# Kernel tuning notes

Measured on AMD Instinct MI355X. Metric: run time of the kernel, lower is better.

The kernel has to match this reference:

```python
import jax, jax.numpy as jnp
import numpy as np

N, C, M = 4096, 176, 131072   # patches per image, feature dim (32+48+96), memory bank size
CHUNK = 8192                  # memory-bank chunk (torch uses 512; same math, fewer scan steps)
TOPK = 10


def setup_inputs() -> dict:
    key = jax.random.key(0)
    k1, k2 = jax.random.split(key)
    return {
        "patch_feats": jax.random.normal(k1, (N, C), dtype=jnp.float32),
        "memory": jax.random.normal(k2, (M, C), dtype=jnp.float32),
        "topk": TOPK,
    }


def reference(patch_feats, memory, topk):
    eps = 1e-6
    # L2-normalize rows (cosine similarity)
    p = patch_feats / (jnp.linalg.norm(patch_feats, axis=1, keepdims=True) + eps)  # [N, C]
    m = memory / (jnp.linalg.norm(memory, axis=1, keepdims=True) + eps)            # [M, C]

    n_chunks = m.shape[0] // CHUNK
    m_chunks = m.reshape(n_chunks, CHUNK, m.shape[1])  # static chunking of memory bank

    def step(carry_min, mb):
        sim = jnp.einsum('nc,kc->nk', p, mb)       # [N, CHUNK] similarity tile
        d = jnp.min(1.0 - sim, axis=1)             # per-chunk min distance, [N]
        return jnp.minimum(carry_min, d), None

    init = jnp.full((p.shape[0],), jnp.inf, dtype=p.dtype)
    patch_scores, _ = jax.lax.scan(step, init, m_chunks)  # running min over chunks

    # image score: mean of top-k patch scores (topk <= N here)
    topk_vals = jax.lax.top_k(patch_scores, topk)[0]
    image_score = jnp.mean(topk_vals)
    return patch_scores, image_score
```

## Files before the change

### kernel.cpp

```cpp
#include <hip/hip_runtime.h>
#include <stdint.h>

typedef unsigned short ushortT;
typedef __bf16 bf16x8 __attribute__((ext_vector_type(8)));
typedef float f32x4 __attribute__((ext_vector_type(4)));
typedef unsigned short ushort8 __attribute__((ext_vector_type(8)));

#define NPATCH 4096
#define MROWS  131072
#define CFEAT  176
#define KST    6
#define TILE_BYTES 6144
#define MSPLIT 48
#define TOT_ITERS 2048
#define BN_TILES 4
#define ITER_BYTES (BN_TILES * TILE_BYTES)
#define LROW 180

__device__ __forceinline__ ushortT f2bf(float f) {
    unsigned u = __float_as_uint(f);
    unsigned r = (u + 0x7FFFu + ((u >> 16) & 1u)) >> 16;
    return (ushortT)r;
}
__device__ __forceinline__ unsigned f2key(float f) {
    unsigned b = __float_as_uint(f);
    return (b & 0x80000000u) ? ~b : (b | 0x80000000u);
}
__device__ __forceinline__ float key2f(unsigned k) {
    return __uint_as_float((k & 0x80000000u) ? (k ^ 0x80000000u) : ~k);
}

__global__ __launch_bounds__(256) void nrmfrag(const float* __restrict__ in,
                                               ushortT* __restrict__ outfr,
                                               unsigned* __restrict__ keys) {
    __shared__ float buf[64 * LROW];
    __shared__ float scale[64];
    const int t = threadIdx.x;
    const int row0 = blockIdx.x * 64;

    if (keys != nullptr && t < 64) keys[blockIdx.x * 64 + t] = 0u;

    const float4* g4 = reinterpret_cast<const float4*>(in + (size_t)row0 * CFEAT);
#pragma unroll
    for (int i = 0; i < 11; ++i) {
        const int idx = i * 256 + t;
        const int row = idx / 44;
        const int c4  = idx - row * 44;
        float4 v = g4[idx];
        *reinterpret_cast<float4*>(&buf[row * LROW + c4 * 4]) = v;
    }
    __syncthreads();

    {
        const int r = t >> 2, part = t & 3;
        const float* rp = &buf[r * LROW + part * 44];
        float s = 0.f;
#pragma unroll
        for (int i = 0; i < 11; ++i) {
            float4 v = *reinterpret_cast<const float4*>(rp + i * 4);
            s += v.x * v.x + v.y * v.y + v.z * v.z + v.w * v.w;
        }
        s += __shfl_xor(s, 1);
        s += __shfl_xor(s, 2);
        if (part == 0) scale[r] = 1.0f / (sqrtf(s) + 1e-6f);
    }
    __syncthreads();

    const int tl = t >> 6;
    const int lane = t & 63;
    const int col = lane & 15, kh = lane >> 4;
    const int lrow = tl * 16 + col;
    const float* rp = &buf[lrow * LROW];
    const float sc = scale[lrow];
    const size_t tile = (size_t)(row0 >> 4) + tl;
#pragma unroll
    for (int ks = 0; ks < KST; ++ks) {
        const int kb = ks * 32 + kh * 8;
        ushort8 o;
        if (kb < CFEAT) {
            float4 v0 = *reinterpret_cast<const float4*>(rp + kb);
            float4 v1 = *reinterpret_cast<const float4*>(rp + kb + 4);
            o[0] = f2bf(v0.x * sc); o[1] = f2bf(v0.y * sc);
            o[2] = f2bf(v0.z * sc); o[3] = f2bf(v0.w * sc);
            o[4] = f2bf(v1.x * sc); o[5] = f2bf(v1.y * sc);
            o[6] = f2bf(v1.z * sc); o[7] = f2bf(v1.w * sc);
        } else {
#pragma unroll
            for (int j = 0; j < 8; ++j) o[j] = 0;
        }
        *reinterpret_cast<ushort8*>(outfr + (tile * KST + ks) * (size_t)512 + lane * 8) = o;
    }
}

__global__ __launch_bounds__(256, 3) void gemm_max(const ushortT* __restrict__ pfr,
                                                   const ushortT* __restrict__ mfr,
                                                   unsigned* __restrict__ keys) {
    __shared__ ushortT lds[2][ITER_BYTES / 2];
    const int t = threadIdx.x;
    const int w = t >> 6;
    const int lane = t & 63;
    const int mchunk = blockIdx.x;
    const int panel = blockIdx.y;

    const int itb = (mchunk * TOT_ITERS) / MSPLIT;
    const int ite = ((mchunk + 1) * TOT_ITERS) / MSPLIT;

    bf16x8 a[4][KST];
    {
        const int ptile0 = panel * 16 + w * 4;
#pragma unroll
        for (int m = 0; m < 4; ++m)
#pragma unroll
            for (int k = 0; k < KST; ++k)
                a[m][k] = *reinterpret_cast<const bf16x8*>(
                    pfr + ((size_t)(ptile0 + m) * KST + k) * 512 + lane * 8);
    }

    float runmax[4][4];
#pragma unroll
    for (int m = 0; m < 4; ++m)
#pragma unroll
        for (int r = 0; r < 4; ++r) runmax[m][r] = -3.0e38f;

    const uint8_t* gb = reinterpret_cast<const uint8_t*>(mfr);

    auto stage = [&](int buf, int it) {
        const uint8_t* src = gb + (size_t)it * ITER_BYTES + w * 6144 + lane * 16;
        uint8_t* dstb = reinterpret_cast<uint8_t*>(&lds[buf][0]) + w * 6144;
#pragma unroll
        for (int i = 0; i < 6; ++i) {
            __builtin_amdgcn_global_load_lds(
                (const __attribute__((address_space(1))) unsigned int*)(src + i * 1024),
                (__attribute__((address_space(3))) unsigned int*)(dstb + i * 1024),
                16, 0, 0);
        }
    };

    stage(0, itb);
    asm volatile("s_waitcnt vmcnt(0)" ::: "memory");
    __builtin_amdgcn_s_barrier();

    int cur = 0;
    for (int it = itb; it < ite; ++it) {
        if (it + 1 < ite) stage(cur ^ 1, it + 1);

        const ushortT* lb = &lds[cur][0];
#pragma unroll
        for (int n = 0; n < BN_TILES; ++n) {
            bf16x8 b[KST];
#pragma unroll
            for (int k = 0; k < KST; ++k)
                b[k] = *reinterpret_cast<const bf16x8*>(lb + (n * KST + k) * 512 + lane * 8);
            f32x4 acc[4];
#pragma unroll
            for (int m = 0; m < 4; ++m) acc[m] = f32x4{0.f, 0.f, 0.f, 0.f};
#pragma unroll
            for (int k = 0; k < KST; ++k)
#pragma unroll
                for (int m = 0; m < 4; ++m)
                    acc[m] = __builtin_amdgcn_mfma_f32_16x16x32_bf16(a[m][k], b[k], acc[m], 0, 0, 0);
#pragma unroll
            for (int m = 0; m < 4; ++m)
#pragma unroll
                for (int r = 0; r < 4; ++r)
                    runmax[m][r] = fmaxf(runmax[m][r], acc[m][r]);
        }

        asm volatile("s_waitcnt vmcnt(0)" ::: "memory");
        __builtin_amdgcn_s_barrier();
        cur ^= 1;
    }

#pragma unroll
    for (int m = 0; m < 4; ++m) {
#pragma unroll
        for (int r = 0; r < 4; ++r) {
            float v = runmax[m][r];
            v = fmaxf(v, __shfl_xor(v, 1));
            v = fmaxf(v, __shfl_xor(v, 2));
            v = fmaxf(v, __shfl_xor(v, 4));
            v = fmaxf(v, __shfl_xor(v, 8));
            if ((lane & 15) == 0) {
                int prow = panel * 256 + w * 64 + m * 16 + (lane >> 4) * 4 + r;
                atomicMax(&keys[prow], f2key(v));
            }
        }
    }
}

__global__ __launch_bounds__(256) void finalize(const unsigned* __restrict__ keys,
                                                const int* __restrict__ topk_p,
                                                float* __restrict__ out) {
    __shared__ float s[NPATCH];
    __shared__ float rv[256];
    __shared__ int ri[256];
    const int t = threadIdx.x;
    for (int i = t; i < NPATCH; i += 256) {
        float score = 1.0f - key2f(keys[i]);
        out[i] = score;
        s[i] = score;
    }
    __syncthreads();
    const int K = *topk_p;
    float sum = 0.f;
    for (int it = 0; it < K; ++it) {
        float bv = -3.0e38f; int bi = -1;
        for (int i = t; i < NPATCH; i += 256)
            if (s[i] > bv) { bv = s[i]; bi = i; }
        rv[t] = bv; ri[t] = bi;
        __syncthreads();
        for (int off = 128; off > 0; off >>= 1) {
            if (t < off && rv[t + off] > rv[t]) { rv[t] = rv[t + off]; ri[t] = ri[t + off]; }
            __syncthreads();
        }
        if (t == 0) { sum += rv[0]; s[ri[0]] = -3.0e38f; }
        __syncthreads();
    }
    if (t == 0) out[NPATCH] = sum / (float)K;
}

extern "C" void kernel_launch(void* const* d_in, const int* in_sizes, int n_in,
                              void* d_out, int out_size, void* d_ws, size_t ws_size,
                              hipStream_t stream) {
    (void)in_sizes; (void)n_in; (void)out_size; (void)ws_size;
    const float* patch = (const float*)d_in[0];
    const float* mem   = (const float*)d_in[1];
    const int*   topk  = (const int*)d_in[2];
    float* out = (float*)d_out;

    uint8_t* ws = (uint8_t*)d_ws;
    ushortT*  mfr  = (ushortT*)ws;
    ushortT*  pfr  = (ushortT*)(ws + 50331648);
    unsigned* keys = (unsigned*)(ws + 50331648 + 1572864);

    nrmfrag<<<MROWS / 64, 256, 0, stream>>>(mem, mfr, nullptr);
    nrmfrag<<<NPATCH / 64, 256, 0, stream>>>(patch, pfr, keys);
    gemm_max<<<dim3(MSPLIT, NPATCH / 256), 256, 0, stream>>>(pfr, mfr, keys);
    finalize<<<1, 256, 0, stream>>>(keys, topk, out);
}
```

Before: 337.2 us.

## Triple-buffer LDS memory tiles and remap grid for XCD-aware chunk scheduling

Moves the GEMM's memory-bank staging from double to triple buffering. Each iteration now waits with a partial vmcnt so loads run two iterations ahead, and a single barrier per iteration replaces the wait-then-barrier at the loop end. The grid becomes 1D with 32 memory chunks of 64 iterations, and block IDs are swizzled so blocks on the same XCD share M-chunks across patch panels, which should improve L2 reuse. Occupancy drops from 3 to 2 blocks per CU, and fewer chunks means fewer blocks in total (512 instead of 768).

```diff
diff --git a/kernel.cpp b/kernel.cpp
--- a/kernel.cpp
+++ b/kernel.cpp
@@ -11,10 +11,10 @@
 #define CFEAT  176
 #define KST    6
 #define TILE_BYTES 6144
-#define MSPLIT 48
-#define TOT_ITERS 2048
+#define MSPLIT 32
 #define BN_TILES 4
 #define ITER_BYTES (BN_TILES * TILE_BYTES)
+#define ITERS 64
 #define LROW 180
 
 __device__ __forceinline__ ushortT f2bf(float f) {
@@ -92,18 +92,22 @@
     }
 }
 
-__global__ __launch_bounds__(256, 3) void gemm_max(const ushortT* __restrict__ pfr,
+__global__ __launch_bounds__(256, 2) void gemm_max(const ushortT* __restrict__ pfr,
                                                    const ushortT* __restrict__ mfr,
                                                    unsigned* __restrict__ keys) {
-    __shared__ ushortT lds[2][ITER_BYTES / 2];
+    __shared__ ushortT lds[3][ITER_BYTES / 2];
     const int t = threadIdx.x;
     const int w = t >> 6;
     const int lane = t & 63;
-    const int mchunk = blockIdx.x;
-    const int panel = blockIdx.y;
-
-    const int itb = (mchunk * TOT_ITERS) / MSPLIT;
-    const int ite = ((mchunk + 1) * TOT_ITERS) / MSPLIT;
+
+    const int bid = blockIdx.x;
+    const int x = bid & 7;
+    const int slot = bid >> 3;
+    const int mchunk = x + 8 * (slot >> 4);
+    const int panel = slot & 15;
+
+    const int itb = mchunk * ITERS;
+    const int ite = itb + ITERS;
 
     bf16x8 a[4][KST];
     {
@@ -137,14 +141,16 @@
     };
 
     stage(0, itb);
-    asm volatile("s_waitcnt vmcnt(0)" ::: "memory");
-    __builtin_amdgcn_s_barrier();
-
-    int cur = 0;
+    stage(1, itb + 1);
+
+    int cb = 0, sb = 2;
     for (int it = itb; it < ite; ++it) {
-        if (it + 1 < ite) stage(cur ^ 1, it + 1);
-
-        const ushortT* lb = &lds[cur][0];
+        if (it + 1 < ite) asm volatile("s_waitcnt vmcnt(6)" ::: "memory");
+        else              asm volatile("s_waitcnt vmcnt(0)" ::: "memory");
+        __builtin_amdgcn_s_barrier();
+        if (it + 2 < ite) stage(sb, it + 2);
+
+        const ushortT* lb = &lds[cb][0];
 #pragma unroll
         for (int n = 0; n < BN_TILES; ++n) {
             bf16x8 b[KST];
@@ -165,10 +171,8 @@
                 for (int r = 0; r < 4; ++r)
                     runmax[m][r] = fmaxf(runmax[m][r], acc[m][r]);
         }
-
-        asm volatile("s_waitcnt vmcnt(0)" ::: "memory");
-        __builtin_amdgcn_s_barrier();
-        cur ^= 1;
+        cb = (cb == 2) ? 0 : cb + 1;
+        sb = (sb == 2) ? 0 : sb + 1;
     }
 
 #pragma unroll
@@ -235,6 +239,6 @@
 
     nrmfrag<<<MROWS / 64, 256, 0, stream>>>(mem, mfr, nullptr);
     nrmfrag<<<NPATCH / 64, 256, 0, stream>>>(patch, pfr, keys);
-    gemm_max<<<dim3(MSPLIT, NPATCH / 256), 256, 0, stream>>>(pfr, mfr, keys);
+    gemm_max<<<MSPLIT * 16, 256, 0, stream>>>(pfr, mfr, keys);
     finalize<<<1, 256, 0, stream>>>(keys, topk, out);
 }
```

Result: faster. 308.2 us (-8.6%).

## Switch GEMM to 32x32x16 bf16 MFMA with matching fragment layout

Applied to the files above, without the earlier changes.

Replaces the 16x16x32 MFMA tiles with 32x32x16 MFMA tiles. The normalize/fragment kernel now writes data in the 32-row, 16-wide K-step layout, and the GEMM uses 2x2 tiles of 32x32 per wave. The M-split drops from 48 to 32 blocks and the occupancy hint drops from 3 to 2. The larger MFMA shape raises operand reuse per instruction, but it brings heavier register pressure (16-float accumulators and 24 A fragments) and fewer resident blocks.

```diff
diff --git a/kernel.cpp b/kernel.cpp
--- a/kernel.cpp
+++ b/kernel.cpp
@@ -3,18 +3,17 @@
 
 typedef unsigned short ushortT;
 typedef __bf16 bf16x8 __attribute__((ext_vector_type(8)));
-typedef float f32x4 __attribute__((ext_vector_type(4)));
+typedef float f32x16 __attribute__((ext_vector_type(16)));
 typedef unsigned short ushort8 __attribute__((ext_vector_type(8)));
 
 #define NPATCH 4096
 #define MROWS  131072
 #define CFEAT  176
-#define KST    6
-#define TILE_BYTES 6144
-#define MSPLIT 48
-#define TOT_ITERS 2048
-#define BN_TILES 4
-#define ITER_BYTES (BN_TILES * TILE_BYTES)
+#define KS32   12
+#define T32_BYTES 12288
+#define MSPLIT 32
+#define ITER_BYTES 24576
+#define ITERS 64
 #define LROW 180
 
 __device__ __forceinline__ ushortT f2bf(float f) {
@@ -66,16 +65,19 @@
     }
     __syncthreads();
 
-    const int tl = t >> 6;
+    const int p = t >> 7;
+    const int half = (t >> 6) & 1;
     const int lane = t & 63;
-    const int col = lane & 15, kh = lane >> 4;
-    const int lrow = tl * 16 + col;
+    const int rit = lane & 31;
+    const int kh = lane >> 5;
+    const int lrow = p * 32 + rit;
     const float* rp = &buf[lrow * LROW];
     const float sc = scale[lrow];
-    const size_t tile = (size_t)(row0 >> 4) + tl;
-#pragma unroll
-    for (int ks = 0; ks < KST; ++ks) {
-        const int kb = ks * 32 + kh * 8;
+    const size_t tile = (size_t)blockIdx.x * 2 + p;
+#pragma unroll
+    for (int i = 0; i < 6; ++i) {
+        const int ks = half + 2 * i;
+        const int kb = ks * 16 + kh * 8;
         ushort8 o;
         if (kb < CFEAT) {
             float4 v0 = *reinterpret_cast<const float4*>(rp + kb);
@@ -88,11 +90,11 @@
 #pragma unroll
             for (int j = 0; j < 8; ++j) o[j] = 0;
         }
-        *reinterpret_cast<ushort8*>(outfr + (tile * KST + ks) * (size_t)512 + lane * 8) = o;
-    }
-}
-
-__global__ __launch_bounds__(256, 3) void gemm_max(const ushortT* __restrict__ pfr,
+        *reinterpret_cast<ushort8*>(outfr + (tile * KS32 + ks) * (size_t)512 + lane * 8) = o;
+    }
+}
+
+__global__ __launch_bounds__(256, 2) void gemm_max(const ushortT* __restrict__ pfr,
                                                    const ushortT* __restrict__ mfr,
                                                    unsigned* __restrict__ keys) {
     __shared__ ushortT lds[2][ITER_BYTES / 2];
@@ -102,25 +104,25 @@
     const int mchunk = blockIdx.x;
     const int panel = blockIdx.y;
 
-    const int itb = (mchunk * TOT_ITERS) / MSPLIT;
-    const int ite = ((mchunk + 1) * TOT_ITERS) / MSPLIT;
-
-    bf16x8 a[4][KST];
+    const int itb = mchunk * ITERS;
+    const int ite = itb + ITERS;
+
+    bf16x8 a[2][KS32];
     {
-        const int ptile0 = panel * 16 + w * 4;
-#pragma unroll
-        for (int m = 0; m < 4; ++m)
-#pragma unroll
-            for (int k = 0; k < KST; ++k)
+        const int ptile0 = panel * 8 + w * 2;
+#pragma unroll
+        for (int m = 0; m < 2; ++m)
+#pragma unroll
+            for (int k = 0; k < KS32; ++k)
                 a[m][k] = *reinterpret_cast<const bf16x8*>(
-                    pfr + ((size_t)(ptile0 + m) * KST + k) * 512 + lane * 8);
-    }
-
-    float runmax[4][4];
-#pragma unroll
-    for (int m = 0; m < 4; ++m)
-#pragma unroll
-        for (int r = 0; r < 4; ++r) runmax[m][r] = -3.0e38f;
+                    pfr + ((size_t)(ptile0 + m) * KS32 + k) * 512 + lane * 8);
+    }
+
+    float runmax[2][16];
+#pragma unroll
+    for (int m = 0; m < 2; ++m)
+#pragma unroll
+        for (int r = 0; r < 16; ++r) runmax[m][r] = -3.0e38f;
 
     const uint8_t* gb = reinterpret_cast<const uint8_t*>(mfr);
 
@@ -146,23 +148,25 @@
 
         const ushortT* lb = &lds[cur][0];
 #pragma unroll
-        for (int n = 0; n < BN_TILES; ++n) {
-            bf16x8 b[KST];
-#pragma unroll
-            for (int k = 0; k < KST; ++k)
-                b[k] = *reinterpret_cast<const bf16x8*>(lb + (n * KST + k) * 512 + lane * 8);
-            f32x4 acc[4];
-#pragma unroll
-            for (int m = 0; m < 4; ++m) acc[m] = f32x4{0.f, 0.f, 0.f, 0.f};
-#pragma unroll
-            for (int k = 0; k < KST; ++k)
-#pragma unroll
-                for (int m = 0; m < 4; ++m)
-                    acc[m] = __builtin_amdgcn_mfma_f32_16x16x32_bf16(a[m][k], b[k], acc[m], 0, 0, 0);
-#pragma unroll
-            for (int m = 0; m < 4; ++m)
-#pragma unroll
-                for (int r = 0; r < 4; ++r)
+        for (int n = 0; n < 2; ++n) {
+            bf16x8 b[KS32];
+#pragma unroll
+            for (int k = 0; k < KS32; ++k)
+                b[k] = *reinterpret_cast<const bf16x8*>(lb + (n * KS32 + k) * 512 + lane * 8);
+            f32x16 acc[2];
+#pragma unroll
+            for (int m = 0; m < 2; ++m)
+#pragma unroll
+                for (int r = 0; r < 16; ++r) acc[m][r] = 0.f;
+#pragma unroll
+            for (int k = 0; k < KS32; ++k)
+#pragma unroll
+                for (int m = 0; m < 2; ++m)
+                    acc[m] = __builtin_amdgcn_mfma_f32_32x32x16_bf16(a[m][k], b[k], acc[m], 0, 0, 0);
+#pragma unroll
+            for (int m = 0; m < 2; ++m)
+#pragma unroll
+                for (int r = 0; r < 16; ++r)
                     runmax[m][r] = fmaxf(runmax[m][r], acc[m][r]);
         }
 
@@ -172,16 +176,18 @@
     }
 
 #pragma unroll
-    for (int m = 0; m < 4; ++m) {
-#pragma unroll
-        for (int r = 0; r < 4; ++r) {
+    for (int m = 0; m < 2; ++m) {
+#pragma unroll
+        for (int r = 0; r < 16; ++r) {
             float v = runmax[m][r];
             v = fmaxf(v, __shfl_xor(v, 1));
             v = fmaxf(v, __shfl_xor(v, 2));
             v = fmaxf(v, __shfl_xor(v, 4));
             v = fmaxf(v, __shfl_xor(v, 8));
-            if ((lane & 15) == 0) {
-                int prow = panel * 256 + w * 64 + m * 16 + (lane >> 4) * 4 + r;
+            v = fmaxf(v, __shfl_xor(v, 16));
+            if ((lane & 31) == 0) {
+                int rowInTile = (r & 3) + 8 * (r >> 2) + 4 * (lane >> 5);
+                int prow = panel * 256 + w * 64 + m * 32 + rowInTile;
                 atomicMax(&keys[prow], f2key(v));
             }
         }
@@ -235,6 +241,6 @@
 
     nrmfrag<<<MROWS / 64, 256, 0, stream>>>(mem, mfr, nullptr);
     nrmfrag<<<NPATCH / 64, 256, 0, stream>>>(patch, pfr, keys);
-    gemm_max<<<dim3(MSPLIT, NPATCH / 256), 256, 0, stream>>>(pfr, mfr, keys);
+    gemm_max<<<dim3(MSPLIT, 16), 256, 0, stream>>>(pfr, mfr, keys);
     finalize<<<1, 256, 0, stream>>>(keys, topk, out);
 }
```

New measurement: 314.7 us. 1.07x faster.

## Use 512-thread GEMM blocks sharing LDS tiles and a shuffle-based top-k finalize

Applied to the files above, without the earlier changes.

The similarity GEMM now runs 8-wave blocks that each cover 512 patch rows, so every memory-bank tile staged into LDS is reused by twice as many waves. Each wave now issues half as many global-to-LDS loads. The split over the memory bank goes from 48 to 64 chunks of fixed 32 iterations, giving a 64x8 grid. The finalize kernel now keeps its scores in registers across 1024 threads and selects the top-k with wave shuffle reductions instead of an LDS tree with many barriers. In exchange, the larger blocks and higher occupancy target raise register pressure, and the grid has fewer blocks.

```diff
diff --git a/kernel.cpp b/kernel.cpp
--- a/kernel.cpp
+++ b/kernel.cpp
@@ -11,10 +11,10 @@
 #define CFEAT  176
 #define KST    6
 #define TILE_BYTES 6144
-#define MSPLIT 48
-#define TOT_ITERS 2048
+#define MSPLIT 64
 #define BN_TILES 4
 #define ITER_BYTES (BN_TILES * TILE_BYTES)
+#define ITERS 32
 #define LROW 180
 
 __device__ __forceinline__ ushortT f2bf(float f) {
@@ -92,7 +92,7 @@
     }
 }
 
-__global__ __launch_bounds__(256, 3) void gemm_max(const ushortT* __restrict__ pfr,
+__global__ __launch_bounds__(512, 4) void gemm_max(const ushortT* __restrict__ pfr,
                                                    const ushortT* __restrict__ mfr,
                                                    unsigned* __restrict__ keys) {
     __shared__ ushortT lds[2][ITER_BYTES / 2];
@@ -102,12 +102,12 @@
     const int mchunk = blockIdx.x;
     const int panel = blockIdx.y;
 
-    const int itb = (mchunk * TOT_ITERS) / MSPLIT;
-    const int ite = ((mchunk + 1) * TOT_ITERS) / MSPLIT;
+    const int itb = mchunk * ITERS;
+    const int ite = itb + ITERS;
 
     bf16x8 a[4][KST];
     {
-        const int ptile0 = panel * 16 + w * 4;
+        const int ptile0 = panel * 32 + w * 4;
 #pragma unroll
         for (int m = 0; m < 4; ++m)
 #pragma unroll
@@ -125,10 +125,10 @@
     const uint8_t* gb = reinterpret_cast<const uint8_t*>(mfr);
 
     auto stage = [&](int buf, int it) {
-        const uint8_t* src = gb + (size_t)it * ITER_BYTES + w * 6144 + lane * 16;
-        uint8_t* dstb = reinterpret_cast<uint8_t*>(&lds[buf][0]) + w * 6144;
-#pragma unroll
-        for (int i = 0; i < 6; ++i) {
+        const uint8_t* src = gb + (size_t)it * ITER_BYTES + w * 3072 + lane * 16;
+        uint8_t* dstb = reinterpret_cast<uint8_t*>(&lds[buf][0]) + w * 3072;
+#pragma unroll
+        for (int i = 0; i < 3; ++i) {
             __builtin_amdgcn_global_load_lds(
                 (const __attribute__((address_space(1))) unsigned int*)(src + i * 1024),
                 (__attribute__((address_space(3))) unsigned int*)(dstb + i * 1024),
@@ -181,40 +181,57 @@
             v = fmaxf(v, __shfl_xor(v, 4));
             v = fmaxf(v, __shfl_xor(v, 8));
             if ((lane & 15) == 0) {
-                int prow = panel * 256 + w * 64 + m * 16 + (lane >> 4) * 4 + r;
+                int prow = panel * 512 + w * 64 + m * 16 + (lane >> 4) * 4 + r;
                 atomicMax(&keys[prow], f2key(v));
             }
         }
     }
 }
 
-__global__ __launch_bounds__(256) void finalize(const unsigned* __restrict__ keys,
-                                                const int* __restrict__ topk_p,
-                                                float* __restrict__ out) {
-    __shared__ float s[NPATCH];
-    __shared__ float rv[256];
-    __shared__ int ri[256];
+__global__ __launch_bounds__(1024) void finalize(const unsigned* __restrict__ keys,
+                                                 const int* __restrict__ topk_p,
+                                                 float* __restrict__ out) {
+    __shared__ float wv[16];
+    __shared__ int wi[16];
+    __shared__ int chosen;
     const int t = threadIdx.x;
-    for (int i = t; i < NPATCH; i += 256) {
-        float score = 1.0f - key2f(keys[i]);
-        out[i] = score;
-        s[i] = score;
-    }
-    __syncthreads();
+    const int lane = t & 63, wid = t >> 6;
+
+    float v[4]; int idx[4];
+#pragma unroll
+    for (int j = 0; j < 4; ++j) {
+        const int i = t + 1024 * j;
+        const float sc = 1.0f - key2f(keys[i]);
+        out[i] = sc;
+        v[j] = sc; idx[j] = i;
+    }
     const int K = *topk_p;
     float sum = 0.f;
-    for (int it = 0; it < K; ++it) {
-        float bv = -3.0e38f; int bi = -1;
-        for (int i = t; i < NPATCH; i += 256)
-            if (s[i] > bv) { bv = s[i]; bi = i; }
-        rv[t] = bv; ri[t] = bi;
+    for (int r = 0; r < K; ++r) {
+        float bv = v[0]; int bi = idx[0];
+#pragma unroll
+        for (int j = 1; j < 4; ++j) if (v[j] > bv) { bv = v[j]; bi = idx[j]; }
+        for (int off = 1; off < 64; off <<= 1) {
+            float ov = __shfl_xor(bv, off);
+            int   oi = __shfl_xor(bi, off);
+            if (ov > bv) { bv = ov; bi = oi; }
+        }
+        if (lane == 0) { wv[wid] = bv; wi[wid] = bi; }
         __syncthreads();
-        for (int off = 128; off > 0; off >>= 1) {
-            if (t < off && rv[t + off] > rv[t]) { rv[t] = rv[t + off]; ri[t] = ri[t + off]; }
-            __syncthreads();
-        }
-        if (t == 0) { sum += rv[0]; s[ri[0]] = -3.0e38f; }
+        if (t < 64) {
+            float xv = (t < 16) ? wv[t] : -3.0e38f;
+            int   xi = (t < 16) ? wi[t] : 0;
+            for (int off = 1; off < 16; off <<= 1) {
+                float ov = __shfl_xor(xv, off);
+                int   oi = __shfl_xor(xi, off);
+                if (ov > xv) { xv = ov; xi = oi; }
+            }
+            if (t == 0) { chosen = xi; sum += xv; }
+        }
         __syncthreads();
+        const int c = chosen;
+#pragma unroll
+        for (int j = 0; j < 4; ++j) if (idx[j] == c) v[j] = -3.0e38f;
     }
     if (t == 0) out[NPATCH] = sum / (float)K;
 }
@@ -235,6 +252,6 @@
 
     nrmfrag<<<MROWS / 64, 256, 0, stream>>>(mem, mfr, nullptr);
     nrmfrag<<<NPATCH / 64, 256, 0, stream>>>(patch, pfr, keys);
-    gemm_max<<<dim3(MSPLIT, NPATCH / 256), 256, 0, stream>>>(pfr, mfr, keys);
-    finalize<<<1, 256, 0, stream>>>(keys, topk, out);
-}
+    gemm_max<<<dim3(MSPLIT, 8), 512, 0, stream>>>(pfr, mfr, keys);
+    finalize<<<1, 1024, 0, stream>>>(keys, topk, out);
+}
```

After: 1.258 ms. 3.73x slower.
